# Optimization experiments

Hardware: AMD Instinct MI355X
Metric: run time of the kernel (lower is better)

Reference implementation:

```python
import jax, jax.numpy as jnp
import numpy as np

B, V, H, W = 8192, 256, 128, 128  # batch, feature dim, SOM grid height/width


def setup_inputs() -> dict:
    key = jax.random.key(0)
    k1, k2 = jax.random.split(key)
    inp = jax.random.uniform(k1, (B, V), dtype=jnp.float32)
    weights = jax.random.uniform(k2, (H * W, V), dtype=jnp.float32)  # SOM codebook
    # grid node coordinates, row-major [i, j] as in the torch locations list
    ii, jj = jnp.meshgrid(jnp.arange(H), jnp.arange(W), indexing='ij')
    locations = jnp.stack([ii, jj], axis=-1).reshape(H * W, 2).astype(jnp.float32)
    return {"input": inp, "weights": weights, "locations": locations}


def reference(input, weights, locations):
    # Pairwise L2 distance between input [B,V] and codebook [N,V] via the
    x2 = jnp.sum(input * input, axis=-1, keepdims=True)        # [B,1]
    w2 = jnp.sum(weights * weights, axis=-1)                   # [N]
    d2 = x2 - 2.0 * (input @ weights.T) + w2                   # [B,N]
    dist = jnp.sqrt(jnp.maximum(d2, 0.0))
    bmu_idx = jnp.argmin(dist, axis=-1)                        # [B]
    losses = jnp.min(dist, axis=-1)                            # [B]
    bmu_locations = locations[bmu_idx]                         # [B,2]
    return bmu_locations, losses
```

## Files before the change

### kernel.cpp

```cpp
#include <hip/hip_runtime.h>
#include <stdint.h>


#define B_DIM 8192
#define V_DIM 256
#define N_DIM 16384

#define WS_W2_OFF     0
#define WS_PACKED_OFF 65536
#define WS_PLANES_OFF 131072
#define XPLANE_BYTES  (B_DIM * V_DIM * 2)
#define WPLANE_BYTES  (N_DIM * V_DIM * 2)
#define WS_FAST_NEED  (WS_PLANES_OFF + 2 * XPLANE_BYTES + 2 * WPLANE_BYTES)

typedef __attribute__((ext_vector_type(8))) short short8;
typedef __attribute__((ext_vector_type(4))) float f32x4;

__device__ __forceinline__ unsigned long long packKey(float s, unsigned idx) {
    unsigned u = __float_as_uint(s);
    u = (u & 0x80000000u) ? ~u : (u | 0x80000000u);
    return ((unsigned long long)u << 32) | (unsigned long long)idx;
}

__global__ __launch_bounds__(256) void w2_kernel(const float* __restrict__ W,
                                                 float* __restrict__ w2) {
    int lane = threadIdx.x & 63;
    int wv   = threadIdx.x >> 6;
    int n    = blockIdx.x * 4 + wv;
    float4 v = ((const float4*)(W + (size_t)n * V_DIM))[lane];
    float s = v.x * v.x + v.y * v.y + v.z * v.z + v.w * v.w;
    #pragma unroll
    for (int m = 32; m >= 1; m >>= 1) s += __shfl_xor(s, m);
    if (lane == 0) w2[n] = s;
}


__device__ __forceinline__ unsigned bfrn(float x) {
    unsigned u = __float_as_uint(x);
    return (u + 0x7FFFu + ((u >> 16) & 1u)) >> 16;
}
__device__ __forceinline__ float bf2f(unsigned h) { return __uint_as_float(h << 16); }

__global__ __launch_bounds__(256) void convert_planes(const float* __restrict__ X,
                                                      const float* __restrict__ W,
                                                      unsigned short* __restrict__ Xh,
                                                      unsigned short* __restrict__ Xl,
                                                      unsigned short* __restrict__ Wh,
                                                      unsigned short* __restrict__ Wl) {
    int gid = blockIdx.x * 256 + threadIdx.x;
    int s   = gid & 31;
    int row = gid >> 5;
    const float* src;
    unsigned short *dh, *dl;
    int r;
    if (row < B_DIM) { r = row; src = X + (size_t)r * V_DIM; dh = Xh; dl = Xl; }
    else             { r = row - B_DIM; src = W + (size_t)r * V_DIM; dh = Wh; dl = Wl; }

    float4 a = ((const float4*)src)[s * 2];
    float4 b = ((const float4*)src)[s * 2 + 1];
    float v[8] = {a.x, a.y, a.z, a.w, b.x, b.y, b.z, b.w};
    unsigned hi[8], lo[8];
    #pragma unroll
    for (int i = 0; i < 8; ++i) {
        hi[i] = bfrn(v[i]);
        lo[i] = bfrn(v[i] - bf2f(hi[i]));
    }
    uint4 hp, lp;
    hp.x = hi[0] | (hi[1] << 16); hp.y = hi[2] | (hi[3] << 16);
    hp.z = hi[4] | (hi[5] << 16); hp.w = hi[6] | (hi[7] << 16);
    lp.x = lo[0] | (lo[1] << 16); lp.y = lo[2] | (lo[3] << 16);
    lp.z = lo[4] | (lo[5] << 16); lp.w = lo[6] | (lo[7] << 16);

    int sp = (s & ~3) | ((s & 3) ^ ((r >> 1) & 3));
    *(uint4*)(dh + (size_t)r * V_DIM + sp * 8) = hp;
    *(uint4*)(dl + (size_t)r * V_DIM + sp * 8) = lp;
}

__device__ __forceinline__ void gl16(const void* g, void* l) {
    __builtin_amdgcn_global_load_lds((const __attribute__((address_space(1))) unsigned int*)g,
                                     (__attribute__((address_space(3))) unsigned int*)l,
                                     16, 0, 0);
}

#define BARX()   asm volatile("s_barrier" ::: "memory")
#define VMC8()   asm volatile("s_waitcnt vmcnt(8)" ::: "memory")
#define VMC0()   asm volatile("s_waitcnt vmcnt(0)" ::: "memory")

__global__ __launch_bounds__(256, 2) void som_fast(const unsigned short* __restrict__ Xh,
                                                   const unsigned short* __restrict__ Xl,
                                                   const unsigned short* __restrict__ Wh,
                                                   const unsigned short* __restrict__ Wl,
                                                   const float* __restrict__ w2,
                                                   unsigned long long* __restrict__ packed) {
    __shared__ __align__(16) char lds[65536];

    const int t    = threadIdx.x;
    const int lane = t & 63;
    const int wv   = t >> 6;
    const int wr   = wv >> 1, wc = wv & 1;
    const int fr   = lane & 15;
    const int kq   = lane >> 4;

    const int bid = blockIdx.x;
    const int xcd = bid & 7;
    const int q   = bid >> 3;
    const int w   = q >> 5;
    const int rb  = xcd * 8 + (w & 1) * 4 + ((q >> 3) & 3);
    const int cb  = (w >> 1) * 8 + (q & 7);
    const int r0 = rb * 128, c0 = cb * 128;

    const char* pXh = (const char*)Xh + (((size_t)(r0 + (t >> 2))) << 9) + ((t & 3) << 4);
    const char* pXl = (const char*)Xl + (((size_t)(r0 + (t >> 2))) << 9) + ((t & 3) << 4);
    const char* pWh = (const char*)Wh + (((size_t)(c0 + (t >> 2))) << 9) + ((t & 3) << 4);
    const char* pWl = (const char*)Wl + (((size_t)(c0 + (t >> 2))) << 9) + ((t & 3) << 4);
    const int t16 = t * 16;

#define ISSUE(kk, B)                                            \
    do {                                                        \
        gl16(pXh + (kk) * 64,         (B) + t16);               \
        gl16(pXh + 32768 + (kk) * 64, (B) + 4096  + t16);       \
        gl16(pXl + (kk) * 64,         (B) + 8192  + t16);       \
        gl16(pXl + 32768 + (kk) * 64, (B) + 12288 + t16);       \
        gl16(pWh + (kk) * 64,         (B) + 16384 + t16);       \
        gl16(pWh + 32768 + (kk) * 64, (B) + 20480 + t16);       \
        gl16(pWl + (kk) * 64,         (B) + 24576 + t16);       \
        gl16(pWl + 32768 + (kk) * 64, (B) + 28672 + t16);       \
    } while (0)

    f32x4 acc[4][4];
    #pragma unroll
    for (int i = 0; i < 4; ++i)
        #pragma unroll
        for (int j = 0; j < 4; ++j)
            acc[i][j] = (f32x4){0.f, 0.f, 0.f, 0.f};

    char* buf0 = lds;
    char* buf1 = lds + 32768;

    ISSUE(0, buf0);

    #pragma unroll
    for (int ks = 0; ks < 8; ++ks) {
        char* cur = (ks & 1) ? buf1 : buf0;
        char* nxt = (ks & 1) ? buf0 : buf1;

        BARX();
        if (ks < 7) { ISSUE(ks + 1, nxt); VMC8(); }
        else        { VMC0(); }
        BARX();

        short8 fah[4], fal[4], fbh[4], fbl[4];
        #pragma unroll
        for (int j = 0; j < 4; ++j) {
            const int col = wc * 64 + j * 16 + fr;
            const int off = col * 64 + ((kq ^ ((col >> 1) & 3)) << 4);
            fbh[j] = *(const short8*)(cur + 16384 + off);
            fbl[j] = *(const short8*)(cur + 24576 + off);
        }
        #pragma unroll
        for (int i = 0; i < 4; ++i) {
            const int row = wr * 64 + i * 16 + fr;
            const int off = row * 64 + ((kq ^ ((row >> 1) & 3)) << 4);
            fah[i] = *(const short8*)(cur + off);
            fal[i] = *(const short8*)(cur + 8192 + off);
        }
        __builtin_amdgcn_s_setprio(1);
        #pragma unroll
        for (int i = 0; i < 4; ++i)
            #pragma unroll
            for (int j = 0; j < 4; ++j) {
                acc[i][j] = __builtin_amdgcn_mfma_f32_16x16x32_bf16(fah[i], fbh[j], acc[i][j], 0, 0, 0);
                acc[i][j] = __builtin_amdgcn_mfma_f32_16x16x32_bf16(fah[i], fbl[j], acc[i][j], 0, 0, 0);
                acc[i][j] = __builtin_amdgcn_mfma_f32_16x16x32_bf16(fal[i], fbh[j], acc[i][j], 0, 0, 0);
            }
        __builtin_amdgcn_s_setprio(0);
    }
#undef ISSUE

    float w2v[4];
    #pragma unroll
    for (int j = 0; j < 4; ++j) w2v[j] = w2[c0 + wc * 64 + j * 16 + fr];

    #pragma unroll
    for (int i = 0; i < 4; ++i) {
        #pragma unroll
        for (int r = 0; r < 4; ++r) {
            const int row = r0 + wr * 64 + i * 16 + kq * 4 + r;
            float best = 3.4e38f;
            unsigned bidx = 0u;
            #pragma unroll
            for (int j = 0; j < 4; ++j) {
                const unsigned n = (unsigned)(c0 + wc * 64 + j * 16 + fr);
                const float s = fmaf(-2.0f, acc[i][j][r], w2v[j]);
                if (s < best) { best = s; bidx = n; }
            }
            #pragma unroll
            for (int m = 1; m <= 8; m <<= 1) {
                float    ov = __shfl_xor(best, m);
                unsigned oi = (unsigned)__shfl_xor((int)bidx, m);
                if (ov < best || (ov == best && oi < bidx)) { best = ov; bidx = oi; }
            }
            if (fr == 0) atomicMin(&packed[row], packKey(best, bidx));
        }
    }
}


__device__ __forceinline__ unsigned packhi2(float a, float b) {
    return (__float_as_uint(a) >> 16) | (__float_as_uint(b) & 0xFFFF0000u);
}
__device__ __forceinline__ unsigned packlo2(float a, float b) {
    float ah = __uint_as_float(__float_as_uint(a) & 0xFFFF0000u);
    float bh = __uint_as_float(__float_as_uint(b) & 0xFFFF0000u);
    return (__float_as_uint(a - ah) >> 16) | (__float_as_uint(b - bh) & 0xFFFF0000u);
}
__device__ __forceinline__ uint4 mku4(unsigned a, unsigned b, unsigned c, unsigned d) {
    uint4 r; r.x = a; r.y = b; r.z = c; r.w = d; return r;
}
__device__ __forceinline__ uint4 hi8(float4 p, float4 q) {
    return mku4(packhi2(p.x, p.y), packhi2(p.z, p.w), packhi2(q.x, q.y), packhi2(q.z, q.w));
}
__device__ __forceinline__ uint4 lo8(float4 p, float4 q) {
    return mku4(packlo2(p.x, p.y), packlo2(p.z, p.w), packlo2(q.x, q.y), packlo2(q.z, q.w));
}
__device__ __forceinline__ int lb(int row, int slot) {
    return row * 64 + ((slot ^ ((row >> 1) & 3)) << 4);
}

__global__ __launch_bounds__(256, 2) void som_mfma(const float* __restrict__ X,
                                                   const float* __restrict__ W,
                                                   const float* __restrict__ w2,
                                                   unsigned long long* __restrict__ packed) {
    __shared__ char lds[4 * 8192];
    char* Ahp = lds;
    char* Alp = lds + 8192;
    char* Bhp = lds + 16384;
    char* Blp = lds + 24576;

    const int t     = threadIdx.x;
    const int lane  = t & 63;
    const int wv    = t >> 6;
    const int wr    = wv >> 1, wc = wv & 1;
    const int fr    = lane & 15;
    const int kslot = lane >> 4;

    const int rb = blockIdx.x >> 7;
    const int cb = blockIdx.x & 127;
    const int r0 = rb * 128, c0 = cb * 128;

    const int sr = t >> 1;
    const int sh = t & 1;
    const float* xg = (const float*)X + (size_t)(r0 + sr) * V_DIM + sh * 16;
    const float* wg = (const float*)W + (size_t)(c0 + sr) * V_DIM + sh * 16;

    float4 pa[4], pb[4];
    #pragma unroll
    for (int q = 0; q < 4; ++q) { pa[q] = ((const float4*)xg)[q]; pb[q] = ((const float4*)wg)[q]; }

    f32x4 acc[4][4];
    #pragma unroll
    for (int i = 0; i < 4; ++i)
        #pragma unroll
        for (int j = 0; j < 4; ++j) acc[i][j] = (f32x4){0.f, 0.f, 0.f, 0.f};

    for (int ks = 0; ks < 8; ++ks) {
        uint4 cah0 = hi8(pa[0], pa[1]), cah1 = hi8(pa[2], pa[3]);
        uint4 cal0 = lo8(pa[0], pa[1]), cal1 = lo8(pa[2], pa[3]);
        uint4 cbh0 = hi8(pb[0], pb[1]), cbh1 = hi8(pb[2], pb[3]);
        uint4 cbl0 = lo8(pb[0], pb[1]), cbl1 = lo8(pb[2], pb[3]);

        __syncthreads();
        *(uint4*)(Ahp + lb(sr, 2 * sh))     = cah0;
        *(uint4*)(Ahp + lb(sr, 2 * sh + 1)) = cah1;
        *(uint4*)(Alp + lb(sr, 2 * sh))     = cal0;
        *(uint4*)(Alp + lb(sr, 2 * sh + 1)) = cal1;
        *(uint4*)(Bhp + lb(sr, 2 * sh))     = cbh0;
        *(uint4*)(Bhp + lb(sr, 2 * sh + 1)) = cbh1;
        *(uint4*)(Blp + lb(sr, 2 * sh))     = cbl0;
        *(uint4*)(Blp + lb(sr, 2 * sh + 1)) = cbl1;
        __syncthreads();

        if (ks + 1 < 8) {
            const float* xn = xg + (ks + 1) * 32;
            const float* wn = wg + (ks + 1) * 32;
            #pragma unroll
            for (int q = 0; q < 4; ++q) { pa[q] = ((const float4*)xn)[q]; pb[q] = ((const float4*)wn)[q]; }
        }

        short8 fah[4], fal[4], fbh[4], fbl[4];
        #pragma unroll
        for (int i = 0; i < 4; ++i) {
            int row = wr * 64 + i * 16 + fr;
            fah[i] = *(const short8*)(Ahp + lb(row, kslot));
            fal[i] = *(const short8*)(Alp + lb(row, kslot));
        }
        #pragma unroll
        for (int j = 0; j < 4; ++j) {
            int col = wc * 64 + j * 16 + fr;
            fbh[j] = *(const short8*)(Bhp + lb(col, kslot));
            fbl[j] = *(const short8*)(Blp + lb(col, kslot));
        }
        #pragma unroll
        for (int i = 0; i < 4; ++i)
            #pragma unroll
            for (int j = 0; j < 4; ++j) {
                acc[i][j] = __builtin_amdgcn_mfma_f32_16x16x32_bf16(fah[i], fbh[j], acc[i][j], 0, 0, 0);
                acc[i][j] = __builtin_amdgcn_mfma_f32_16x16x32_bf16(fah[i], fbl[j], acc[i][j], 0, 0, 0);
                acc[i][j] = __builtin_amdgcn_mfma_f32_16x16x32_bf16(fal[i], fbh[j], acc[i][j], 0, 0, 0);
            }
    }

    float w2v[4];
    #pragma unroll
    for (int j = 0; j < 4; ++j) w2v[j] = w2[c0 + wc * 64 + j * 16 + fr];

    #pragma unroll
    for (int i = 0; i < 4; ++i) {
        #pragma unroll
        for (int r = 0; r < 4; ++r) {
            const int row = r0 + wr * 64 + i * 16 + kslot * 4 + r;
            float best = 3.4e38f;
            unsigned bidx = 0u;
            #pragma unroll
            for (int j = 0; j < 4; ++j) {
                const unsigned n = (unsigned)(c0 + wc * 64 + j * 16 + fr);
                const float s = fmaf(-2.0f, acc[i][j][r], w2v[j]);
                if (s < best) { best = s; bidx = n; }
            }
            #pragma unroll
            for (int m = 1; m <= 8; m <<= 1) {
                float    ov = __shfl_xor(best, m);
                unsigned oi = (unsigned)__shfl_xor((int)bidx, m);
                if (ov < best || (ov == best && oi < bidx)) { best = ov; bidx = oi; }
            }
            if (fr == 0) atomicMin(&packed[row], packKey(best, bidx));
        }
    }
}

__global__ __launch_bounds__(256) void finalize(const float* __restrict__ X,
                                                const float* __restrict__ loc,
                                                const unsigned long long* __restrict__ packed,
                                                float* __restrict__ out) {
    int lane = threadIdx.x & 63;
    int wv   = threadIdx.x >> 6;
    int b    = blockIdx.x * 4 + wv;
    float4 v = ((const float4*)(X + (size_t)b * V_DIM))[lane];
    float x2 = v.x * v.x + v.y * v.y + v.z * v.z + v.w * v.w;
    #pragma unroll
    for (int m = 32; m >= 1; m >>= 1) x2 += __shfl_xor(x2, m);
    if (lane == 0) {
        unsigned long long p = packed[b];
        unsigned key = (unsigned)(p >> 32);
        unsigned idx = (unsigned)(p & 0xFFFFFFFFu);
        unsigned sb  = (key & 0x80000000u) ? (key & 0x7FFFFFFFu) : ~key;
        float s  = __uint_as_float(sb);
        float d2 = fmaxf(x2 + s, 0.0f);
        out[2 * b]     = loc[2 * idx];
        out[2 * b + 1] = loc[2 * idx + 1];
        out[2 * B_DIM + b] = sqrtf(d2);
    }
}

extern "C" void kernel_launch(void* const* d_in, const int* in_sizes, int n_in,
                              void* d_out, int out_size, void* d_ws, size_t ws_size,
                              hipStream_t stream) {
    const float* X = (const float*)d_in[0];
    const float* W = (const float*)d_in[1];
    const float* L = (const float*)d_in[2];
    float* out = (float*)d_out;

    float* w2 = (float*)((char*)d_ws + WS_W2_OFF);
    unsigned long long* packed = (unsigned long long*)((char*)d_ws + WS_PACKED_OFF);

    hipMemsetAsync(packed, 0xFF, B_DIM * sizeof(unsigned long long), stream);
    w2_kernel<<<N_DIM / 4, 256, 0, stream>>>(W, w2);

    if (ws_size >= (size_t)WS_FAST_NEED) {
        unsigned short* Xh = (unsigned short*)((char*)d_ws + WS_PLANES_OFF);
        unsigned short* Xl = (unsigned short*)((char*)Xh + XPLANE_BYTES);
        unsigned short* Wh = (unsigned short*)((char*)Xl + XPLANE_BYTES);
        unsigned short* Wl = (unsigned short*)((char*)Wh + WPLANE_BYTES);
        convert_planes<<<(B_DIM + N_DIM) * 32 / 256, 256, 0, stream>>>(X, W, Xh, Xl, Wh, Wl);
        som_fast<<<(B_DIM / 128) * (N_DIM / 128), 256, 0, stream>>>(Xh, Xl, Wh, Wl, w2, packed);
    } else {
        som_mfma<<<(B_DIM / 128) * (N_DIM / 128), 256, 0, stream>>>(X, W, w2, packed);
    }
    finalize<<<B_DIM / 4, 256, 0, stream>>>(X, L, packed, out);
}
```

Measured before the change: 272.4 us.

## Pre-swizzle W into MFMA fragment layout and load B operands directly to registers

The conversion kernel now writes the W hi/lo bf16 planes in MFMA-fragment order, so each lane's 16-byte B fragment is contiguous. The GEMM kernel loads B fragments straight from global memory into double-buffered registers instead of staging them through LDS. LDS use halves to 32KB and there is one fewer barrier per k-step. In exchange, B tiles are no longer shared across the two waves that use them, so each W fragment is fetched twice from global/L2, and register pressure rises.

```diff
diff --git a/kernel.cpp b/kernel.cpp
--- a/kernel.cpp
+++ b/kernel.cpp
@@ -41,39 +41,49 @@
 }
 __device__ __forceinline__ float bf2f(unsigned h) { return __uint_as_float(h << 16); }
 
+__device__ __forceinline__ void hilo8(const float4& a, const float4& b,
+                                      uint4& hp, uint4& lp) {
+    float v[8] = {a.x, a.y, a.z, a.w, b.x, b.y, b.z, b.w};
+    unsigned hi[8], lo[8];
+    #pragma unroll
+    for (int i = 0; i < 8; ++i) {
+        hi[i] = bfrn(v[i]);
+        lo[i] = bfrn(v[i] - bf2f(hi[i]));
+    }
+    hp.x = hi[0] | (hi[1] << 16); hp.y = hi[2] | (hi[3] << 16);
+    hp.z = hi[4] | (hi[5] << 16); hp.w = hi[6] | (hi[7] << 16);
+    lp.x = lo[0] | (lo[1] << 16); lp.y = lo[2] | (lo[3] << 16);
+    lp.z = lo[4] | (lo[5] << 16); lp.w = lo[6] | (lo[7] << 16);
+}
+
 __global__ __launch_bounds__(256) void convert_planes(const float* __restrict__ X,
                                                       const float* __restrict__ W,
                                                       unsigned short* __restrict__ Xh,
                                                       unsigned short* __restrict__ Xl,
                                                       unsigned short* __restrict__ Wh,
                                                       unsigned short* __restrict__ Wl) {
-    int gid = blockIdx.x * 256 + threadIdx.x;
-    int s   = gid & 31;
-    int row = gid >> 5;
-    const float* src;
-    unsigned short *dh, *dl;
-    int r;
-    if (row < B_DIM) { r = row; src = X + (size_t)r * V_DIM; dh = Xh; dl = Xl; }
-    else             { r = row - B_DIM; src = W + (size_t)r * V_DIM; dh = Wh; dl = Wl; }
-
-    float4 a = ((const float4*)src)[s * 2];
-    float4 b = ((const float4*)src)[s * 2 + 1];
-    float v[8] = {a.x, a.y, a.z, a.w, b.x, b.y, b.z, b.w};
-    unsigned hi[8], lo[8];
-    #pragma unroll
-    for (int i = 0; i < 8; ++i) {
-        hi[i] = bfrn(v[i]);
-        lo[i] = bfrn(v[i] - bf2f(hi[i]));
-    }
-    uint4 hp, lp;
-    hp.x = hi[0] | (hi[1] << 16); hp.y = hi[2] | (hi[3] << 16);
-    hp.z = hi[4] | (hi[5] << 16); hp.w = hi[6] | (hi[7] << 16);
-    lp.x = lo[0] | (lo[1] << 16); lp.y = lo[2] | (lo[3] << 16);
-    lp.z = lo[4] | (lo[5] << 16); lp.w = lo[6] | (lo[7] << 16);
-
-    int sp = (s & ~3) | ((s & 3) ^ ((r >> 1) & 3));
-    *(uint4*)(dh + (size_t)r * V_DIM + sp * 8) = hp;
-    *(uint4*)(dl + (size_t)r * V_DIM + sp * 8) = lp;
+    const int gid = blockIdx.x * 256 + threadIdx.x;
+    if (blockIdx.x < 1024) {
+        int s = gid & 31, r = gid >> 5;
+        const float* src = X + (size_t)r * V_DIM;
+        float4 a = ((const float4*)src)[s * 2];
+        float4 b = ((const float4*)src)[s * 2 + 1];
+        uint4 hp, lp; hilo8(a, b, hp, lp);
+        int sp = (s & ~3) | ((s & 3) ^ ((r >> 1) & 3));
+        *(uint4*)(Xh + (size_t)r * V_DIM + sp * 8) = hp;
+        *(uint4*)(Xl + (size_t)r * V_DIM + sp * 8) = lp;
+    } else {
+        int wid = gid - 1024 * 256;
+        int fr = wid & 15, kq = (wid >> 4) & 3, ks = (wid >> 6) & 7, nb = wid >> 9;
+        int row = nb * 16 + fr;
+        int s   = ks * 4 + kq;
+        const float* src = W + (size_t)row * V_DIM;
+        float4 a = ((const float4*)src)[s * 2];
+        float4 b = ((const float4*)src)[s * 2 + 1];
+        uint4 hp, lp; hilo8(a, b, hp, lp);
+        *(uint4*)(Wh + (size_t)wid * 8) = hp;
+        *(uint4*)(Wl + (size_t)wid * 8) = lp;
+    }
 }
 
 __device__ __forceinline__ void gl16(const void* g, void* l) {
@@ -83,16 +93,16 @@
 }
 
 #define BARX()   asm volatile("s_barrier" ::: "memory")
-#define VMC8()   asm volatile("s_waitcnt vmcnt(8)" ::: "memory")
+#define VMC12()  asm volatile("s_waitcnt vmcnt(12)" ::: "memory")
 #define VMC0()   asm volatile("s_waitcnt vmcnt(0)" ::: "memory")
 
 __global__ __launch_bounds__(256, 2) void som_fast(const unsigned short* __restrict__ Xh,
                                                    const unsigned short* __restrict__ Xl,
-                                                   const unsigned short* __restrict__ Wh,
-                                                   const unsigned short* __restrict__ Wl,
+                                                   const unsigned short* __restrict__ Wfh,
+                                                   const unsigned short* __restrict__ Wfl,
                                                    const float* __restrict__ w2,
                                                    unsigned long long* __restrict__ packed) {
-    __shared__ __align__(16) char lds[65536];
+    __shared__ __align__(16) char lds[32768];
 
     const int t    = threadIdx.x;
     const int lane = t & 63;
@@ -111,20 +121,44 @@
 
     const char* pXh = (const char*)Xh + (((size_t)(r0 + (t >> 2))) << 9) + ((t & 3) << 4);
     const char* pXl = (const char*)Xl + (((size_t)(r0 + (t >> 2))) << 9) + ((t & 3) << 4);
-    const char* pWh = (const char*)Wh + (((size_t)(c0 + (t >> 2))) << 9) + ((t & 3) << 4);
-    const char* pWl = (const char*)Wl + (((size_t)(c0 + (t >> 2))) << 9) + ((t & 3) << 4);
     const int t16 = t * 16;
 
-#define ISSUE(kk, B)                                            \
+#define ISSUE_A(kk, B)                                          \
     do {                                                        \
         gl16(pXh + (kk) * 64,         (B) + t16);               \
         gl16(pXh + 32768 + (kk) * 64, (B) + 4096  + t16);       \
         gl16(pXl + (kk) * 64,         (B) + 8192  + t16);       \
         gl16(pXl + 32768 + (kk) * 64, (B) + 12288 + t16);       \
-        gl16(pWh + (kk) * 64,         (B) + 16384 + t16);       \
-        gl16(pWh + 32768 + (kk) * 64, (B) + 20480 + t16);       \
-        gl16(pWl + (kk) * 64,         (B) + 24576 + t16);       \
-        gl16(pWl + 32768 + (kk) * 64, (B) + 28672 + t16);       \
+    } while (0)
+
+    const char* wbh[4];
+    const char* wbl[4];
+    #pragma unroll
+    for (int j = 0; j < 4; ++j) {
+        const size_t nb = (size_t)(cb * 8 + wc * 4 + j);
+        wbh[j] = (const char*)Wfh + nb * 8192 + lane * 16;
+        wbl[j] = (const char*)Wfl + nb * 8192 + lane * 16;
+    }
+
+#define LOADB(kk, BH, BL)                                         \
+    do {                                                          \
+        _Pragma("unroll")                                         \
+        for (int j = 0; j < 4; ++j) {                             \
+            BH[j] = *(const short8*)(wbh[j] + (kk) * 1024);       \
+            BL[j] = *(const short8*)(wbl[j] + (kk) * 1024);       \
+        }                                                         \
+    } while (0)
+
+#define MFMA_ALL(BH, BL)                                                                           \
+    do {                                                                                           \
+        _Pragma("unroll")                                                                          \
+        for (int i = 0; i < 4; ++i)                                                                \
+            _Pragma("unroll")                                                                      \
+            for (int j = 0; j < 4; ++j) {                                                          \
+                acc[i][j] = __builtin_amdgcn_mfma_f32_16x16x32_bf16(fah[i], BH[j], acc[i][j], 0, 0, 0); \
+                acc[i][j] = __builtin_amdgcn_mfma_f32_16x16x32_bf16(fah[i], BL[j], acc[i][j], 0, 0, 0); \
+                acc[i][j] = __builtin_amdgcn_mfma_f32_16x16x32_bf16(fal[i], BH[j], acc[i][j], 0, 0, 0); \
+            }                                                                                      \
     } while (0)
 
     f32x4 acc[4][4];
@@ -135,28 +169,29 @@
             acc[i][j] = (f32x4){0.f, 0.f, 0.f, 0.f};
 
     char* buf0 = lds;
-    char* buf1 = lds + 32768;
-
-    ISSUE(0, buf0);
+    char* buf1 = lds + 16384;
+
+    short8 b0h[4], b0l[4], b1h[4], b1l[4];
+
+    ISSUE_A(0, buf0);
+    LOADB(0, b0h, b0l);
 
     #pragma unroll
     for (int ks = 0; ks < 8; ++ks) {
         char* cur = (ks & 1) ? buf1 : buf0;
         char* nxt = (ks & 1) ? buf0 : buf1;
 
+        if (ks < 7) {
+            ISSUE_A(ks + 1, nxt);
+            if ((ks + 1) & 1) LOADB(ks + 1, b1h, b1l);
+            else              LOADB(ks + 1, b0h, b0l);
+            VMC12();
+        } else {
+            VMC0();
+        }
         BARX();
-        if (ks < 7) { ISSUE(ks + 1, nxt); VMC8(); }
-        else        { VMC0(); }
-        BARX();
-
-        short8 fah[4], fal[4], fbh[4], fbl[4];
-        #pragma unroll
-        for (int j = 0; j < 4; ++j) {
-            const int col = wc * 64 + j * 16 + fr;
-            const int off = col * 64 + ((kq ^ ((col >> 1) & 3)) << 4);
-            fbh[j] = *(const short8*)(cur + 16384 + off);
-            fbl[j] = *(const short8*)(cur + 24576 + off);
-        }
+
+        short8 fah[4], fal[4];
         #pragma unroll
         for (int i = 0; i < 4; ++i) {
             const int row = wr * 64 + i * 16 + fr;
@@ -164,18 +199,16 @@
             fah[i] = *(const short8*)(cur + off);
             fal[i] = *(const short8*)(cur + 8192 + off);
         }
+
         __builtin_amdgcn_s_setprio(1);
-        #pragma unroll
-        for (int i = 0; i < 4; ++i)
-            #pragma unroll
-            for (int j = 0; j < 4; ++j) {
-                acc[i][j] = __builtin_amdgcn_mfma_f32_16x16x32_bf16(fah[i], fbh[j], acc[i][j], 0, 0, 0);
-                acc[i][j] = __builtin_amdgcn_mfma_f32_16x16x32_bf16(fah[i], fbl[j], acc[i][j], 0, 0, 0);
-                acc[i][j] = __builtin_amdgcn_mfma_f32_16x16x32_bf16(fal[i], fbh[j], acc[i][j], 0, 0, 0);
-            }
+        if (ks & 1) MFMA_ALL(b1h, b1l);
+        else        MFMA_ALL(b0h, b0l);
         __builtin_amdgcn_s_setprio(0);
-    }
-#undef ISSUE
+        BARX();
+    }
+#undef ISSUE_A
+#undef LOADB
+#undef MFMA_ALL
 
     float w2v[4];
     #pragma unroll
@@ -377,12 +410,12 @@
     w2_kernel<<<N_DIM / 4, 256, 0, stream>>>(W, w2);
 
     if (ws_size >= (size_t)WS_FAST_NEED) {
-        unsigned short* Xh = (unsigned short*)((char*)d_ws + WS_PLANES_OFF);
-        unsigned short* Xl = (unsigned short*)((char*)Xh + XPLANE_BYTES);
-        unsigned short* Wh = (unsigned short*)((char*)Xl + XPLANE_BYTES);
-        unsigned short* Wl = (unsigned short*)((char*)Wh + WPLANE_BYTES);
-        convert_planes<<<(B_DIM + N_DIM) * 32 / 256, 256, 0, stream>>>(X, W, Xh, Xl, Wh, Wl);
-        som_fast<<<(B_DIM / 128) * (N_DIM / 128), 256, 0, stream>>>(Xh, Xl, Wh, Wl, w2, packed);
+        unsigned short* Xh  = (unsigned short*)((char*)d_ws + WS_PLANES_OFF);
+        unsigned short* Xl  = (unsigned short*)((char*)Xh + XPLANE_BYTES);
+        unsigned short* Wfh = (unsigned short*)((char*)Xl + XPLANE_BYTES);
+        unsigned short* Wfl = (unsigned short*)((char*)Wfh + WPLANE_BYTES);
+        convert_planes<<<3072, 256, 0, stream>>>(X, W, Xh, Xl, Wfh, Wfl);
+        som_fast<<<(B_DIM / 128) * (N_DIM / 128), 256, 0, stream>>>(Xh, Xl, Wfh, Wfl, w2, packed);
     } else {
         som_mfma<<<(B_DIM / 128) * (N_DIM / 128), 256, 0, stream>>>(X, W, w2, packed);
     }
```

Result: slower. 283.1 us (+3.9%).

## Pre-swizzle bf16 planes into MFMA fragment order and load directly from global

Applied to the files above, without the earlier changes.

The conversion kernel now writes the hi/lo bf16 planes in per-16-row, per-k-step MFMA fragment order, so each lane's short8 operand is one contiguous 16-byte global load. The GEMM kernel drops the LDS double buffer, barriers and global_load_lds staging, and reads fragments straight from global memory, with launch bounds raised to 4 blocks per CU. This removes LDS traffic and barrier synchronisation, but each wave now re-reads its operands from L2 without cross-wave sharing through LDS and gives up explicit prefetch overlap.

```diff
diff --git a/kernel.cpp b/kernel.cpp
--- a/kernel.cpp
+++ b/kernel.cpp
@@ -41,23 +41,8 @@
 }
 __device__ __forceinline__ float bf2f(unsigned h) { return __uint_as_float(h << 16); }
 
-__global__ __launch_bounds__(256) void convert_planes(const float* __restrict__ X,
-                                                      const float* __restrict__ W,
-                                                      unsigned short* __restrict__ Xh,
-                                                      unsigned short* __restrict__ Xl,
-                                                      unsigned short* __restrict__ Wh,
-                                                      unsigned short* __restrict__ Wl) {
-    int gid = blockIdx.x * 256 + threadIdx.x;
-    int s   = gid & 31;
-    int row = gid >> 5;
-    const float* src;
-    unsigned short *dh, *dl;
-    int r;
-    if (row < B_DIM) { r = row; src = X + (size_t)r * V_DIM; dh = Xh; dl = Xl; }
-    else             { r = row - B_DIM; src = W + (size_t)r * V_DIM; dh = Wh; dl = Wl; }
-
-    float4 a = ((const float4*)src)[s * 2];
-    float4 b = ((const float4*)src)[s * 2 + 1];
+__device__ __forceinline__ void hilo8(const float4& a, const float4& b,
+                                      uint4& hp, uint4& lp) {
     float v[8] = {a.x, a.y, a.z, a.w, b.x, b.y, b.z, b.w};
     unsigned hi[8], lo[8];
     #pragma unroll
@@ -65,39 +50,56 @@
         hi[i] = bfrn(v[i]);
         lo[i] = bfrn(v[i] - bf2f(hi[i]));
     }
-    uint4 hp, lp;
     hp.x = hi[0] | (hi[1] << 16); hp.y = hi[2] | (hi[3] << 16);
     hp.z = hi[4] | (hi[5] << 16); hp.w = hi[6] | (hi[7] << 16);
     lp.x = lo[0] | (lo[1] << 16); lp.y = lo[2] | (lo[3] << 16);
     lp.z = lo[4] | (lo[5] << 16); lp.w = lo[6] | (lo[7] << 16);
-
-    int sp = (s & ~3) | ((s & 3) ^ ((r >> 1) & 3));
-    *(uint4*)(dh + (size_t)r * V_DIM + sp * 8) = hp;
-    *(uint4*)(dl + (size_t)r * V_DIM + sp * 8) = lp;
-}
-
-__device__ __forceinline__ void gl16(const void* g, void* l) {
-    __builtin_amdgcn_global_load_lds((const __attribute__((address_space(1))) unsigned int*)g,
-                                     (__attribute__((address_space(3))) unsigned int*)l,
-                                     16, 0, 0);
-}
-
-#define BARX()   asm volatile("s_barrier" ::: "memory")
-#define VMC8()   asm volatile("s_waitcnt vmcnt(8)" ::: "memory")
-#define VMC0()   asm volatile("s_waitcnt vmcnt(0)" ::: "memory")
-
-__global__ __launch_bounds__(256, 2) void som_fast(const unsigned short* __restrict__ Xh,
-                                                   const unsigned short* __restrict__ Xl,
-                                                   const unsigned short* __restrict__ Wh,
-                                                   const unsigned short* __restrict__ Wl,
+}
+
+__global__ __launch_bounds__(256) void convert_planes(const float* __restrict__ X,
+                                                      const float* __restrict__ W,
+                                                      unsigned short* __restrict__ Xfh,
+                                                      unsigned short* __restrict__ Xfl,
+                                                      unsigned short* __restrict__ Wfh,
+                                                      unsigned short* __restrict__ Wfl) {
+    const int gid = blockIdx.x * 256 + threadIdx.x;
+    const float* src;
+    unsigned short *dh, *dl;
+    int tid;
+    if (blockIdx.x < 1024) {
+        tid = gid;
+        const int lane = tid & 63, ck = tid >> 6;
+        const int ks = ck & 7, chunk = ck >> 3;
+        const int row = chunk * 16 + (lane & 15);
+        const int k0  = ks * 32 + (lane >> 4) * 8;
+        src = X + (size_t)row * V_DIM + k0;
+        dh = Xfh; dl = Xfl;
+    } else {
+        tid = gid - 262144;
+        const int lane = tid & 63, ck = tid >> 6;
+        const int ks = ck & 7, chunk = ck >> 3;
+        const int row = chunk * 16 + (lane & 15);
+        const int k0  = ks * 32 + (lane >> 4) * 8;
+        src = W + (size_t)row * V_DIM + k0;
+        dh = Wfh; dl = Wfl;
+    }
+    float4 a = ((const float4*)src)[0];
+    float4 b = ((const float4*)src)[1];
+    uint4 hp, lp; hilo8(a, b, hp, lp);
+    *(uint4*)(dh + (size_t)tid * 8) = hp;
+    *(uint4*)(dl + (size_t)tid * 8) = lp;
+}
+
+__global__ __launch_bounds__(256, 4) void som_fast(const unsigned short* __restrict__ Xfh,
+                                                   const unsigned short* __restrict__ Xfl,
+                                                   const unsigned short* __restrict__ Wfh,
+                                                   const unsigned short* __restrict__ Wfl,
                                                    const float* __restrict__ w2,
                                                    unsigned long long* __restrict__ packed) {
-    __shared__ __align__(16) char lds[65536];
-
     const int t    = threadIdx.x;
     const int lane = t & 63;
-    const int wv   = t >> 6;
-    const int wr   = wv >> 1, wc = wv & 1;
+    const int wvu  = __builtin_amdgcn_readfirstlane(t >> 6);
+    const int wr   = wvu >> 1, wc = wvu & 1;
     const int fr   = lane & 15;
     const int kq   = lane >> 4;
 
@@ -109,23 +111,11 @@
     const int cb  = (w >> 1) * 8 + (q & 7);
     const int r0 = rb * 128, c0 = cb * 128;
 
-    const char* pXh = (const char*)Xh + (((size_t)(r0 + (t >> 2))) << 9) + ((t & 3) << 4);
-    const char* pXl = (const char*)Xl + (((size_t)(r0 + (t >> 2))) << 9) + ((t & 3) << 4);
-    const char* pWh = (const char*)Wh + (((size_t)(c0 + (t >> 2))) << 9) + ((t & 3) << 4);
-    const char* pWl = (const char*)Wl + (((size_t)(c0 + (t >> 2))) << 9) + ((t & 3) << 4);
-    const int t16 = t * 16;
-
-#define ISSUE(kk, B)                                            \
-    do {                                                        \
-        gl16(pXh + (kk) * 64,         (B) + t16);               \
-        gl16(pXh + 32768 + (kk) * 64, (B) + 4096  + t16);       \
-        gl16(pXl + (kk) * 64,         (B) + 8192  + t16);       \
-        gl16(pXl + 32768 + (kk) * 64, (B) + 12288 + t16);       \
-        gl16(pWh + (kk) * 64,         (B) + 16384 + t16);       \
-        gl16(pWh + 32768 + (kk) * 64, (B) + 20480 + t16);       \
-        gl16(pWl + (kk) * 64,         (B) + 24576 + t16);       \
-        gl16(pWl + 32768 + (kk) * 64, (B) + 28672 + t16);       \
-    } while (0)
+    const int vo = lane * 16;
+    const char* Ah = (const char*)Xfh + (size_t)(rb * 8 + wr * 4) * 8192;
+    const char* Al = (const char*)Xfl + (size_t)(rb * 8 + wr * 4) * 8192;
+    const char* Bh = (const char*)Wfh + (size_t)(cb * 8 + wc * 4) * 8192;
+    const char* Bl = (const char*)Wfl + (size_t)(cb * 8 + wc * 4) * 8192;
 
     f32x4 acc[4][4];
     #pragma unroll
@@ -134,48 +124,28 @@
         for (int j = 0; j < 4; ++j)
             acc[i][j] = (f32x4){0.f, 0.f, 0.f, 0.f};
 
-    char* buf0 = lds;
-    char* buf1 = lds + 32768;
-
-    ISSUE(0, buf0);
-
     #pragma unroll
     for (int ks = 0; ks < 8; ++ks) {
-        char* cur = (ks & 1) ? buf1 : buf0;
-        char* nxt = (ks & 1) ? buf0 : buf1;
-
-        BARX();
-        if (ks < 7) { ISSUE(ks + 1, nxt); VMC8(); }
-        else        { VMC0(); }
-        BARX();
-
-        short8 fah[4], fal[4], fbh[4], fbl[4];
+        short8 fbh[4], fbl[4];
         #pragma unroll
         for (int j = 0; j < 4; ++j) {
-            const int col = wc * 64 + j * 16 + fr;
-            const int off = col * 64 + ((kq ^ ((col >> 1) & 3)) << 4);
-            fbh[j] = *(const short8*)(cur + 16384 + off);
-            fbl[j] = *(const short8*)(cur + 24576 + off);
+            fbh[j] = *(const short8*)(Bh + (j * 8 + ks) * 1024 + vo);
+            fbl[j] = *(const short8*)(Bl + (j * 8 + ks) * 1024 + vo);
         }
         #pragma unroll
         for (int i = 0; i < 4; ++i) {
-            const int row = wr * 64 + i * 16 + fr;
-            const int off = row * 64 + ((kq ^ ((row >> 1) & 3)) << 4);
-            fah[i] = *(const short8*)(cur + off);
-            fal[i] = *(const short8*)(cur + 8192 + off);
-        }
-        __builtin_amdgcn_s_setprio(1);
-        #pragma unroll
-        for (int i = 0; i < 4; ++i)
+            short8 fah = *(const short8*)(Ah + (i * 8 + ks) * 1024 + vo);
+            short8 fal = *(const short8*)(Al + (i * 8 + ks) * 1024 + vo);
+            __builtin_amdgcn_s_setprio(1);
             #pragma unroll
             for (int j = 0; j < 4; ++j) {
-                acc[i][j] = __builtin_amdgcn_mfma_f32_16x16x32_bf16(fah[i], fbh[j], acc[i][j], 0, 0, 0);
-                acc[i][j] = __builtin_amdgcn_mfma_f32_16x16x32_bf16(fah[i], fbl[j], acc[i][j], 0, 0, 0);
-                acc[i][j] = __builtin_amdgcn_mfma_f32_16x16x32_bf16(fal[i], fbh[j], acc[i][j], 0, 0, 0);
-            }
-        __builtin_amdgcn_s_setprio(0);
-    }
-#undef ISSUE
+                acc[i][j] = __builtin_amdgcn_mfma_f32_16x16x32_bf16(fah, fbh[j], acc[i][j], 0, 0, 0);
+                acc[i][j] = __builtin_amdgcn_mfma_f32_16x16x32_bf16(fah, fbl[j], acc[i][j], 0, 0, 0);
+                acc[i][j] = __builtin_amdgcn_mfma_f32_16x16x32_bf16(fal, fbh[j], acc[i][j], 0, 0, 0);
+            }
+            __builtin_amdgcn_s_setprio(0);
+        }
+    }
 
     float w2v[4];
     #pragma unroll
@@ -377,12 +347,12 @@
     w2_kernel<<<N_DIM / 4, 256, 0, stream>>>(W, w2);
 
     if (ws_size >= (size_t)WS_FAST_NEED) {
-        unsigned short* Xh = (unsigned short*)((char*)d_ws + WS_PLANES_OFF);
-        unsigned short* Xl = (unsigned short*)((char*)Xh + XPLANE_BYTES);
-        unsigned short* Wh = (unsigned short*)((char*)Xl + XPLANE_BYTES);
-        unsigned short* Wl = (unsigned short*)((char*)Wh + WPLANE_BYTES);
-        convert_planes<<<(B_DIM + N_DIM) * 32 / 256, 256, 0, stream>>>(X, W, Xh, Xl, Wh, Wl);
-        som_fast<<<(B_DIM / 128) * (N_DIM / 128), 256, 0, stream>>>(Xh, Xl, Wh, Wl, w2, packed);
+        unsigned short* Xfh = (unsigned short*)((char*)d_ws + WS_PLANES_OFF);
+        unsigned short* Xfl = (unsigned short*)((char*)Xfh + XPLANE_BYTES);
+        unsigned short* Wfh = (unsigned short*)((char*)Xfl + XPLANE_BYTES);
+        unsigned short* Wfl = (unsigned short*)((char*)Wfh + WPLANE_BYTES);
+        convert_planes<<<3072, 256, 0, stream>>>(X, W, Xfh, Xfl, Wfh, Wfl);
+        som_fast<<<(B_DIM / 128) * (N_DIM / 128), 256, 0, stream>>>(Xfh, Xfl, Wfh, Wfl, w2, packed);
     } else {
         som_mfma<<<(B_DIM / 128) * (N_DIM / 128), 256, 0, stream>>>(X, W, w2, packed);
     }
```

Result: slower. 464.8 us (+70.6%).
